# Performance work log

Measured on AMD Instinct MI355X. Metric: run time of the kernel, lower is better.

The kernel has to match this reference:

```python
import jax, jax.numpy as jnp
import numpy as np


def _gaussian_kernel(ksize: int, sigma: float) -> jnp.ndarray:
    # Normalized 2-D Gaussian, matching get_gaussian_kernel(ksize, sigma).
    r = jnp.arange(ksize, dtype=jnp.float32) - (ksize - 1) / 2.0
    g = jnp.exp(-(r ** 2) / (2.0 * sigma ** 2))
    k2 = jnp.outer(g, g)
    return k2 / jnp.sum(k2)


def setup_inputs() -> dict:
    key = jax.random.key(0)
    x = jax.random.normal(key, (4, 1, 2048, 2048), dtype=jnp.float32)
    # Sobel filters (ImageGradientsLayer): Ix, Iy. Shape (2, 1, 3, 3) OIHW.
    sx = jnp.array([[-1., 0., 1.], [-2., 0., 2.], [-1., 0., 1.]], dtype=jnp.float32)
    sy = sx.T
    sobel_w = jnp.stack([sx, sy])[:, None]  # (2,1,3,3)
    # Depthwise Gaussian conv weight shared across 3 channels: (3,1,7,7)
    KSIZE, SIGMA = 7, 5.0
    gk = _gaussian_kernel(KSIZE, SIGMA)
    gauss_w = jnp.tile(gk[None, None], (3, 1, 1, 1))
    return {"x": x, "sobel_w": sobel_w, "gauss_w": gauss_w}


def reference(x, sobel_w, gauss_w):
    dn = ("NCHW", "OIHW", "NCHW")
    # ImageGradientsLayer: Sobel conv, padding 1 -> (N,2,H,W)
    grads = jax.lax.conv_general_dilated(x, sobel_w, (1, 1), [(1, 1), (1, 1)],
                                         dimension_numbers=dn)
    Ix, Iy = grads[:, 0], grads[:, 1]
    # ChannelProductLayer: (N,3,H,W) = [I_xx, I_yy, I_xy]
    prods = jnp.stack([Ix * Ix, Iy * Iy, Ix * Iy], axis=1)
    # SecondMomentMatrixLayer: same 7x7 Gaussian applied per channel (depthwise)
    S = jax.lax.conv_general_dilated(prods, gauss_w, (1, 1), [(3, 3), (3, 3)],
                                     dimension_numbers=dn, feature_group_count=3)
    # NMSLayer: global lower-median threshold (torch.median semantics),
    # 7x7 stride-1 maxpool (implicit -inf padding like nn.MaxPool2d),
    # equality mask, multiply back.
    med = jnp.quantile(S, 0.5, method="lower")
    xt = jnp.where(S > med, S, jnp.zeros((), S.dtype))
    y = jax.lax.reduce_window(xt, -jnp.inf, jax.lax.max,
                              (1, 1, 7, 7), (1, 1, 1, 1),
                              [(0, 0), (0, 0), (3, 3), (3, 3)])
    mask = (xt == y).astype(xt.dtype)
    return mask * xt
```

## Files before the change

### kernel.cpp

```cpp
#include <hip/hip_runtime.h>
#include <math.h>

#define HH 2048
#define WW 2048
#define NIMG 4
#define NCH 3
#define PLANES (NIMG*NCH)
#define PIX (HH*WW)
#define TOT (PLANES*PIX)
#define W4 (WW/4)
#define MED_RANK 25165823u

struct GW { float w[7]; };

#define H1C 64
#define H23C 16
__device__ unsigned g_hist1p[H1C * 256];
__device__ unsigned g_hist2p[H23C * 4096];
__device__ unsigned g_hist3p[H23C * 4096];
__device__ unsigned g_ctrl[8];
__device__ float    g_med;

__global__ void zero_state() {
    int t = blockIdx.x * 256 + threadIdx.x;
    if (t < H1C * 256) g_hist1p[t] = 0;
    g_hist2p[t] = 0;
    g_hist3p[t] = 0;
    if (t < 8) g_ctrl[t] = 0;
    if (t == 0) g_med = 0.f;
}

__device__ __forceinline__ unsigned f2key(float f) {
    unsigned b = __float_as_uint(f);
    return (b & 0x80000000u) ? ~b : (b | 0x80000000u);
}

#define HCOPY 8
#define HSTRIDE 257

struct RLE {
    unsigned cur, cnt;
    __device__ __forceinline__ void init() { cur = 0xFFFFFFFFu; cnt = 0; }
    __device__ __forceinline__ void add(unsigned* myh, unsigned b) {
        if (b == cur) { cnt++; }
        else { if (cnt) atomicAdd(&myh[cur], cnt); cur = b; cnt = 1; }
    }
    __device__ __forceinline__ void flush(unsigned* myh) {
        if (cnt) atomicAdd(&myh[cur], cnt);
    }
};

#define TX 32
#define TY 64
__global__ __launch_bounds__(256) void sobel_gauss_full(const float* __restrict__ x,
                                                        float* __restrict__ S, GW g) {
    __shared__ float xs[72][40];
    __shared__ float bh[3][70][36];
    __shared__ unsigned lh[HCOPY * HSTRIDE];
    for (int i = threadIdx.x; i < HCOPY * HSTRIDE; i += 256) lh[i] = 0;
    unsigned* myh = lh + (threadIdx.x & (HCOPY - 1)) * HSTRIDE;

    int bx = blockIdx.x * TX, by = blockIdx.y * TY;
    int n = blockIdx.z;
    const float* xp = x + (size_t)n * PIX;
    int t = threadIdx.x;

    for (int i = t; i < 72 * 10; i += 256) {
        int r = i / 10, cc = i % 10;
        int gr = by - 4 + r, gc = bx - 4 + cc * 4;
        float4 v = make_float4(0, 0, 0, 0);
        if (gr >= 0 && gr < HH && gc >= 0 && gc < WW)
            v = *(const float4*)(xp + (size_t)gr * WW + gc);
        *(float4*)&xs[r][cc * 4] = v;
    }
    __syncthreads();

    for (int i = t; i < 70 * 8; i += 256) {
        int r = i >> 3, c = i & 7;
        int imgrow = by - 3 + r;
        if (imgrow < 0 || imgrow >= HH) {
            float4 z = make_float4(0, 0, 0, 0);
            *(float4*)&bh[0][r][4 * c] = z;
            *(float4*)&bh[1][r][4 * c] = z;
            *(float4*)&bh[2][r][4 * c] = z;
            continue;
        }
        float r0[12], r1[12], r2[12];
#pragma unroll
        for (int b = 0; b < 3; b++) {
            float4 v0 = *(float4*)&xs[r][4 * c + 4 * b];
            float4 v1 = *(float4*)&xs[r + 1][4 * c + 4 * b];
            float4 v2 = *(float4*)&xs[r + 2][4 * c + 4 * b];
            r0[b*4+0]=v0.x; r0[b*4+1]=v0.y; r0[b*4+2]=v0.z; r0[b*4+3]=v0.w;
            r1[b*4+0]=v1.x; r1[b*4+1]=v1.y; r1[b*4+2]=v1.z; r1[b*4+3]=v1.w;
            r2[b*4+0]=v2.x; r2[b*4+1]=v2.y; r2[b*4+2]=v2.z; r2[b*4+3]=v2.w;
        }
        float pxx[10], pyy[10], pxy[10];
#pragma unroll
        for (int p = 0; p < 10; p++) {
            int ai = p + 1;
            int cg = bx + 4 * c - 3 + p;
            float Ix = (r0[ai+1] - r0[ai-1]) + 2.f*(r1[ai+1] - r1[ai-1]) + (r2[ai+1] - r2[ai-1]);
            float Iy = (r2[ai-1] - r0[ai-1]) + 2.f*(r2[ai]   - r0[ai])   + (r2[ai+1] - r0[ai+1]);
            bool ok = (cg >= 0 && cg < WW);
            pxx[p] = ok ? Ix * Ix : 0.f;
            pyy[p] = ok ? Iy * Iy : 0.f;
            pxy[p] = ok ? Ix * Iy : 0.f;
        }
        float4 oxx, oyy, oxy;
        float* ox = &oxx.x; float* oy = &oyy.x; float* oz = &oxy.x;
#pragma unroll
        for (int k = 0; k < 4; k++) {
            float sxx = 0.f, syy = 0.f, sxy = 0.f;
#pragma unroll
            for (int j = 0; j < 7; j++) {
                sxx += g.w[j] * pxx[k + j];
                syy += g.w[j] * pyy[k + j];
                sxy += g.w[j] * pxy[k + j];
            }
            ox[k] = sxx; oy[k] = syy; oz[k] = sxy;
        }
        *(float4*)&bh[0][r][4 * c] = oxx;
        *(float4*)&bh[1][r][4 * c] = oyy;
        *(float4*)&bh[2][r][4 * c] = oxy;
    }
    __syncthreads();

    int cg = t & 7, ro0 = (t >> 3) * 2;
    RLE rle; rle.init();
#pragma unroll
    for (int ch = 0; ch < 3; ch++) {
        float4 w[8];
#pragma unroll
        for (int j = 0; j < 8; j++) w[j] = *(float4*)&bh[ch][ro0 + j][4 * cg];
        float4 a0 = make_float4(0, 0, 0, 0), a1 = a0;
#pragma unroll
        for (int j = 0; j < 7; j++) {
            float gw = g.w[j];
            a0.x += gw * w[j].x;   a0.y += gw * w[j].y;
            a0.z += gw * w[j].z;   a0.w += gw * w[j].w;
            a1.x += gw * w[j+1].x; a1.y += gw * w[j+1].y;
            a1.z += gw * w[j+1].z; a1.w += gw * w[j+1].w;
        }
        float* sp = S + (size_t)(n * NCH + ch) * PIX;
        *(float4*)(sp + (size_t)(by + ro0)     * WW + bx + 4 * cg) = a0;
        *(float4*)(sp + (size_t)(by + ro0 + 1) * WW + bx + 4 * cg) = a1;
        rle.add(myh, f2key(a0.x) >> 24); rle.add(myh, f2key(a0.y) >> 24);
        rle.add(myh, f2key(a0.z) >> 24); rle.add(myh, f2key(a0.w) >> 24);
        rle.add(myh, f2key(a1.x) >> 24); rle.add(myh, f2key(a1.y) >> 24);
        rle.add(myh, f2key(a1.z) >> 24); rle.add(myh, f2key(a1.w) >> 24);
    }
    rle.flush(myh);

    __syncthreads();
    if (threadIdx.x < 256) {
        unsigned v = 0;
#pragma unroll
        for (int c = 0; c < HCOPY; c++) v += lh[c * HSTRIDE + threadIdx.x];
        if (v) atomicAdd(&g_hist1p[((blockIdx.y * 64 + blockIdx.x) & (H1C - 1)) * 256 + threadIdx.x], v);
    }
}

#define SCAN_BLOCKS 2048
#define NSTR 8
#define SLAB (TOT / 4 / NSTR)
__global__ __launch_bounds__(256) void hist_mid(const float* __restrict__ S) {
    __shared__ unsigned lh[4096];
    for (int i = threadIdx.x; i < 4096; i += 256) lh[i] = 0;
    __syncthreads();
    unsigned b1 = g_ctrl[0];
    const float4* S4 = (const float4*)S;
    long long i0 = (long long)blockIdx.x * 256 + threadIdx.x;
    const long long STRIDE = (long long)SCAN_BLOCKS * 256;
    float4 v[3][NSTR];
#pragma unroll
    for (int it = 0; it < 3; it++)
#pragma unroll
        for (int s = 0; s < NSTR; s++)
            v[it][s] = S4[i0 + it * STRIDE + (long long)s * SLAB];
#pragma unroll
    for (int it = 0; it < 3; it++)
#pragma unroll
        for (int s = 0; s < NSTR; s++) {
            unsigned k0 = f2key(v[it][s].x), k1 = f2key(v[it][s].y),
                     k2 = f2key(v[it][s].z), k3 = f2key(v[it][s].w);
            if ((k0 >> 24) == b1) atomicAdd(&lh[(k0 >> 12) & 0xFFFu], 1u);
            if ((k1 >> 24) == b1) atomicAdd(&lh[(k1 >> 12) & 0xFFFu], 1u);
            if ((k2 >> 24) == b1) atomicAdd(&lh[(k2 >> 12) & 0xFFFu], 1u);
            if ((k3 >> 24) == b1) atomicAdd(&lh[(k3 >> 12) & 0xFFFu], 1u);
        }
    __syncthreads();
    unsigned cpy = (blockIdx.x & (H23C - 1)) * 4096;
    for (int i = threadIdx.x; i < 4096; i += 256) {
        unsigned vv = lh[i];
        if (vv) atomicAdd(&g_hist2p[cpy + i], vv);
    }
}

__global__ __launch_bounds__(256) void hist_low(const float* __restrict__ S) {
    __shared__ unsigned lh[4096];
    for (int i = threadIdx.x; i < 4096; i += 256) lh[i] = 0;
    __syncthreads();
    unsigned p2 = (g_ctrl[0] << 12) | g_ctrl[1];
    const float4* S4 = (const float4*)S;
    long long i0 = (long long)blockIdx.x * 256 + threadIdx.x;
    const long long STRIDE = (long long)SCAN_BLOCKS * 256;
    float4 v[3][NSTR];
#pragma unroll
    for (int it = 0; it < 3; it++)
#pragma unroll
        for (int s = 0; s < NSTR; s++)
            v[it][s] = S4[i0 + it * STRIDE + (long long)s * SLAB];
#pragma unroll
    for (int it = 0; it < 3; it++)
#pragma unroll
        for (int s = 0; s < NSTR; s++) {
            unsigned k0 = f2key(v[it][s].x), k1 = f2key(v[it][s].y),
                     k2 = f2key(v[it][s].z), k3 = f2key(v[it][s].w);
            if ((k0 >> 12) == p2) atomicAdd(&lh[k0 & 0xFFFu], 1u);
            if ((k1 >> 12) == p2) atomicAdd(&lh[k1 & 0xFFFu], 1u);
            if ((k2 >> 12) == p2) atomicAdd(&lh[k2 & 0xFFFu], 1u);
            if ((k3 >> 12) == p2) atomicAdd(&lh[k3 & 0xFFFu], 1u);
        }
    __syncthreads();
    unsigned cpy = (blockIdx.x & (H23C - 1)) * 4096;
    for (int i = threadIdx.x; i < 4096; i += 256) {
        unsigned vv = lh[i];
        if (vv) atomicAdd(&g_hist3p[cpy + i], vv);
    }
}

__global__ __launch_bounds__(256) void select_k(int which) {
    __shared__ unsigned cnt[4096];
    __shared__ unsigned csum[256];
    int t = threadIdx.x;
    int nbins = (which == 0) ? 256 : 4096;
    if (which == 0) {
        unsigned s = 0;
        for (int c = 0; c < H1C; c++) s += g_hist1p[c * 256 + t];
        cnt[t] = s;
    } else {
        const unsigned* hp = (which == 1) ? g_hist2p : g_hist3p;
        for (int i = t; i < 4096; i += 256) {
            unsigned s = 0;
            for (int c = 0; c < H23C; c++) s += hp[c * 4096 + i];
            cnt[i] = s;
        }
    }
    __syncthreads();
    int per = nbins >> 8;
    unsigned s = 0;
    for (int j = 0; j < per; j++) s += cnt[t * per + j];
    csum[t] = s;
    __syncthreads();
    if (t == 0) {
        unsigned r = (which == 0) ? MED_RANK : (which == 1) ? g_ctrl[3] : g_ctrl[4];
        unsigned acc = 0; int c = 0;
        for (; c < 256; c++) { if (acc + csum[c] > r) break; acc += csum[c]; }
        int b = c * per;
        for (;; b++) { if (acc + cnt[b] > r) break; acc += cnt[b]; }
        if (which == 0)      { g_ctrl[0] = (unsigned)b; g_ctrl[3] = r - acc; }
        else if (which == 1) { g_ctrl[1] = (unsigned)b; g_ctrl[4] = r - acc; }
        else {
            g_ctrl[2] = (unsigned)b;
            unsigned key = (g_ctrl[0] << 24) | (g_ctrl[1] << 12) | (unsigned)b;
            unsigned bits = (key & 0x80000000u) ? (key ^ 0x80000000u) : ~key;
            g_med = __uint_as_float(bits);
        }
    }
}

#define OX 64
#define OY 16
__global__ __launch_bounds__(256) void nms_kernel(const float* __restrict__ S,
                                                  float* __restrict__ out) {
    __shared__ float tin[22][72];
    __shared__ float hm[22][68];
    float med = g_med;
    int plane = blockIdx.z;
    int bx = blockIdx.x * OX, by = blockIdx.y * OY;
    const float* Sp = S + (size_t)plane * PIX;
    int t = threadIdx.x;

    for (int i = t; i < 22 * 18; i += 256) {
        int r = i / 18, cc = i % 18;
        int ghh = by + r - 3;
        int gc  = bx - 4 + cc * 4;
        float4 v = make_float4(-INFINITY, -INFINITY, -INFINITY, -INFINITY);
        if (ghh >= 0 && ghh < HH && gc >= 0 && gc < WW) {
            float4 s = *(const float4*)(Sp + (size_t)ghh * WW + gc);
            v.x = (s.x > med) ? s.x : 0.f;
            v.y = (s.y > med) ? s.y : 0.f;
            v.z = (s.z > med) ? s.z : 0.f;
            v.w = (s.w > med) ? s.w : 0.f;
        }
        *(float4*)&tin[r][cc * 4] = v;
    }
    __syncthreads();

    for (int i = t; i < 22 * 16; i += 256) {
        int r = i / 16, c = i % 16;
        float a0 = tin[r][4*c+1], a1 = tin[r][4*c+2], a2 = tin[r][4*c+3];
        float a3 = tin[r][4*c+4], a4 = tin[r][4*c+5], a5 = tin[r][4*c+6];
        float a6 = tin[r][4*c+7], a7 = tin[r][4*c+8], a8 = tin[r][4*c+9];
        float a9 = tin[r][4*c+10];
        float m03 = fmaxf(fmaxf(a0, a1), fmaxf(a2, a3));
        float m36 = fmaxf(fmaxf(a3, a4), fmaxf(a5, a6));
        float4 o;
        o.x = fmaxf(m03, fmaxf(fmaxf(a4, a5), a6));
        o.y = fmaxf(fmaxf(a1, a2), fmaxf(m36, a7));
        o.z = fmaxf(fmaxf(a2, a3), fmaxf(fmaxf(a4, m36), fmaxf(a7, a8)));
        o.w = fmaxf(m36, fmaxf(fmaxf(a7, a8), a9));
        *(float4*)&hm[r][4*c] = o;
    }
    __syncthreads();

    int cc = t & 15, ro = t >> 4;
    float4 m = *(const float4*)&hm[ro][4*cc];
#pragma unroll
    for (int d = 1; d < 7; d++) {
        float4 h = *(const float4*)&hm[ro + d][4*cc];
        m.x = fmaxf(m.x, h.x); m.y = fmaxf(m.y, h.y);
        m.z = fmaxf(m.z, h.z); m.w = fmaxf(m.w, h.w);
    }
    float4 c0 = *(const float4*)&tin[ro + 3][4*cc + 4];
    float4 o;
    o.x = (c0.x == m.x) ? c0.x : 0.f;
    o.y = (c0.y == m.y) ? c0.y : 0.f;
    o.z = (c0.z == m.z) ? c0.z : 0.f;
    o.w = (c0.w == m.w) ? c0.w : 0.f;
    *(float4*)(out + (size_t)plane * PIX + (size_t)(by + ro) * WW + bx + 4*cc) = o;
}

extern "C" void kernel_launch(void* const* d_in, const int* in_sizes, int n_in,
                              void* d_out, int out_size, void* d_ws, size_t ws_size,
                              hipStream_t stream) {
    const float* x = (const float*)d_in[0];
    float* O = (float*)d_out;
    float* W = (float*)d_ws;

    GW g;
    {
        double gg[7], s = 0.0;
        for (int i = 0; i < 7; i++) { double r = i - 3.0; gg[i] = exp(-r * r / 50.0); s += gg[i]; }
        for (int i = 0; i < 7; i++) g.w[i] = (float)(gg[i] / s);
    }

    zero_state<<<256, 256, 0, stream>>>();
    sobel_gauss_full<<<dim3(WW / TX, HH / TY, NIMG), 256, 0, stream>>>(x, W, g);
    select_k<<<1, 256, 0, stream>>>(0);
    hist_mid<<<SCAN_BLOCKS, 256, 0, stream>>>(W);
    select_k<<<1, 256, 0, stream>>>(1);
    hist_low<<<SCAN_BLOCKS, 256, 0, stream>>>(W);
    select_k<<<1, 256, 0, stream>>>(2);
    nms_kernel<<<dim3(WW / OX, HH / OY, PLANES), 256, 0, stream>>>(W, O);
}
```

Before: 513.8 us.

## Shrink conv tile, alias histogram onto input tile, and flatten histogram scan kernels

```diff
diff --git a/kernel.cpp b/kernel.cpp
--- a/kernel.cpp
+++ b/kernel.cpp
@@ -35,7 +35,7 @@
     return (b & 0x80000000u) ? ~b : (b | 0x80000000u);
 }
 
-#define HCOPY 8
+#define HCOPY 4
 #define HSTRIDE 257
 
 struct RLE {
@@ -51,21 +51,19 @@
 };
 
 #define TX 32
-#define TY 64
+#define TY 32
 __global__ __launch_bounds__(256) void sobel_gauss_full(const float* __restrict__ x,
                                                         float* __restrict__ S, GW g) {
-    __shared__ float xs[72][40];
-    __shared__ float bh[3][70][36];
-    __shared__ unsigned lh[HCOPY * HSTRIDE];
-    for (int i = threadIdx.x; i < HCOPY * HSTRIDE; i += 256) lh[i] = 0;
-    unsigned* myh = lh + (threadIdx.x & (HCOPY - 1)) * HSTRIDE;
+    __shared__ float xs[40][40];
+    __shared__ float bh[3][38][36];
+    unsigned* lh = (unsigned*)&xs[0][0];
 
     int bx = blockIdx.x * TX, by = blockIdx.y * TY;
     int n = blockIdx.z;
     const float* xp = x + (size_t)n * PIX;
     int t = threadIdx.x;
 
-    for (int i = t; i < 72 * 10; i += 256) {
+    for (int i = t; i < 40 * 10; i += 256) {
         int r = i / 10, cc = i % 10;
         int gr = by - 4 + r, gc = bx - 4 + cc * 4;
         float4 v = make_float4(0, 0, 0, 0);
@@ -75,7 +73,7 @@
     }
     __syncthreads();
 
-    for (int i = t; i < 70 * 8; i += 256) {
+    for (int i = t; i < 38 * 8; i += 256) {
         int r = i >> 3, c = i & 7;
         int imgrow = by - 3 + r;
         if (imgrow < 0 || imgrow >= HH) {
@@ -126,29 +124,28 @@
     }
     __syncthreads();
 
-    int cg = t & 7, ro0 = (t >> 3) * 2;
+    for (int i = t; i < HCOPY * HSTRIDE; i += 256) lh[i] = 0;
+    __syncthreads();
+    unsigned* myh = lh + (threadIdx.x & (HCOPY - 1)) * HSTRIDE;
+
+    int cg = t & 7, ro = t >> 3;
     RLE rle; rle.init();
 #pragma unroll
     for (int ch = 0; ch < 3; ch++) {
-        float4 w[8];
-#pragma unroll
-        for (int j = 0; j < 8; j++) w[j] = *(float4*)&bh[ch][ro0 + j][4 * cg];
-        float4 a0 = make_float4(0, 0, 0, 0), a1 = a0;
+        float4 w[7];
+#pragma unroll
+        for (int j = 0; j < 7; j++) w[j] = *(float4*)&bh[ch][ro + j][4 * cg];
+        float4 a0 = make_float4(0, 0, 0, 0);
 #pragma unroll
         for (int j = 0; j < 7; j++) {
             float gw = g.w[j];
-            a0.x += gw * w[j].x;   a0.y += gw * w[j].y;
-            a0.z += gw * w[j].z;   a0.w += gw * w[j].w;
-            a1.x += gw * w[j+1].x; a1.y += gw * w[j+1].y;
-            a1.z += gw * w[j+1].z; a1.w += gw * w[j+1].w;
+            a0.x += gw * w[j].x; a0.y += gw * w[j].y;
+            a0.z += gw * w[j].z; a0.w += gw * w[j].w;
         }
         float* sp = S + (size_t)(n * NCH + ch) * PIX;
-        *(float4*)(sp + (size_t)(by + ro0)     * WW + bx + 4 * cg) = a0;
-        *(float4*)(sp + (size_t)(by + ro0 + 1) * WW + bx + 4 * cg) = a1;
+        *(float4*)(sp + (size_t)(by + ro) * WW + bx + 4 * cg) = a0;
         rle.add(myh, f2key(a0.x) >> 24); rle.add(myh, f2key(a0.y) >> 24);
         rle.add(myh, f2key(a0.z) >> 24); rle.add(myh, f2key(a0.w) >> 24);
-        rle.add(myh, f2key(a1.x) >> 24); rle.add(myh, f2key(a1.y) >> 24);
-        rle.add(myh, f2key(a1.z) >> 24); rle.add(myh, f2key(a1.w) >> 24);
     }
     rle.flush(myh);
 
@@ -161,7 +158,7 @@
     }
 }
 
-#define SCAN_BLOCKS 2048
+#define SCAN_BLOCKS 6144
 #define NSTR 8
 #define SLAB (TOT / 4 / NSTR)
 __global__ __launch_bounds__(256) void hist_mid(const float* __restrict__ S) {
@@ -171,24 +168,18 @@
     unsigned b1 = g_ctrl[0];
     const float4* S4 = (const float4*)S;
     long long i0 = (long long)blockIdx.x * 256 + threadIdx.x;
-    const long long STRIDE = (long long)SCAN_BLOCKS * 256;
-    float4 v[3][NSTR];
-#pragma unroll
-    for (int it = 0; it < 3; it++)
-#pragma unroll
-        for (int s = 0; s < NSTR; s++)
-            v[it][s] = S4[i0 + it * STRIDE + (long long)s * SLAB];
-#pragma unroll
-    for (int it = 0; it < 3; it++)
-#pragma unroll
-        for (int s = 0; s < NSTR; s++) {
-            unsigned k0 = f2key(v[it][s].x), k1 = f2key(v[it][s].y),
-                     k2 = f2key(v[it][s].z), k3 = f2key(v[it][s].w);
-            if ((k0 >> 24) == b1) atomicAdd(&lh[(k0 >> 12) & 0xFFFu], 1u);
-            if ((k1 >> 24) == b1) atomicAdd(&lh[(k1 >> 12) & 0xFFFu], 1u);
-            if ((k2 >> 24) == b1) atomicAdd(&lh[(k2 >> 12) & 0xFFFu], 1u);
-            if ((k3 >> 24) == b1) atomicAdd(&lh[(k3 >> 12) & 0xFFFu], 1u);
-        }
+    float4 v[NSTR];
+#pragma unroll
+    for (int s = 0; s < NSTR; s++) v[s] = S4[i0 + (long long)s * SLAB];
+#pragma unroll
+    for (int s = 0; s < NSTR; s++) {
+        unsigned k0 = f2key(v[s].x), k1 = f2key(v[s].y),
+                 k2 = f2key(v[s].z), k3 = f2key(v[s].w);
+        if ((k0 >> 24) == b1) atomicAdd(&lh[(k0 >> 12) & 0xFFFu], 1u);
+        if ((k1 >> 24) == b1) atomicAdd(&lh[(k1 >> 12) & 0xFFFu], 1u);
+        if ((k2 >> 24) == b1) atomicAdd(&lh[(k2 >> 12) & 0xFFFu], 1u);
+        if ((k3 >> 24) == b1) atomicAdd(&lh[(k3 >> 12) & 0xFFFu], 1u);
+    }
     __syncthreads();
     unsigned cpy = (blockIdx.x & (H23C - 1)) * 4096;
     for (int i = threadIdx.x; i < 4096; i += 256) {
@@ -204,24 +195,18 @@
     unsigned p2 = (g_ctrl[0] << 12) | g_ctrl[1];
     const float4* S4 = (const float4*)S;
     long long i0 = (long long)blockIdx.x * 256 + threadIdx.x;
-    const long long STRIDE = (long long)SCAN_BLOCKS * 256;
-    float4 v[3][NSTR];
-#pragma unroll
-    for (int it = 0; it < 3; it++)
-#pragma unroll
-        for (int s = 0; s < NSTR; s++)
-            v[it][s] = S4[i0 + it * STRIDE + (long long)s * SLAB];
-#pragma unroll
-    for (int it = 0; it < 3; it++)
-#pragma unroll
-        for (int s = 0; s < NSTR; s++) {
-            unsigned k0 = f2key(v[it][s].x), k1 = f2key(v[it][s].y),
-                     k2 = f2key(v[it][s].z), k3 = f2key(v[it][s].w);
-            if ((k0 >> 12) == p2) atomicAdd(&lh[k0 & 0xFFFu], 1u);
-            if ((k1 >> 12) == p2) atomicAdd(&lh[k1 & 0xFFFu], 1u);
-            if ((k2 >> 12) == p2) atomicAdd(&lh[k2 & 0xFFFu], 1u);
-            if ((k3 >> 12) == p2) atomicAdd(&lh[k3 & 0xFFFu], 1u);
-        }
+    float4 v[NSTR];
+#pragma unroll
+    for (int s = 0; s < NSTR; s++) v[s] = S4[i0 + (long long)s * SLAB];
+#pragma unroll
+    for (int s = 0; s < NSTR; s++) {
+        unsigned k0 = f2key(v[s].x), k1 = f2key(v[s].y),
+                 k2 = f2key(v[s].z), k3 = f2key(v[s].w);
+        if ((k0 >> 12) == p2) atomicAdd(&lh[k0 & 0xFFFu], 1u);
+        if ((k1 >> 12) == p2) atomicAdd(&lh[k1 & 0xFFFu], 1u);
+        if ((k2 >> 12) == p2) atomicAdd(&lh[k2 & 0xFFFu], 1u);
+        if ((k3 >> 12) == p2) atomicAdd(&lh[k3 & 0xFFFu], 1u);
+    }
     __syncthreads();
     unsigned cpy = (blockIdx.x & (H23C - 1)) * 4096;
     for (int i = threadIdx.x; i < 4096; i += 256) {
```

Result: slower. 529.9 us (+3.1%).
